# Kernel optimization log

Measured on AMD Instinct MI355X. Metric: run time of the kernel, lower is better.

## Reference

```python
import jax, jax.numpy as jnp
import numpy as np

N = 50000      # nodes
T = 4          # snapshots
F_IN = 128     # in_channels
H_DIM = 128    # hidden_channels
E = 800000     # edges per snapshot
K = 3          # Chebyshev order


def _edge_norm(src, dst, n):
    # PyG ChebConv sym normalization with lambda_max=2.0:
    # L_hat = L - I = -D^{-1/2} A D^{-1/2}  (diagonal of L_hat is 0)
    ones = jnp.ones(src.shape[0], jnp.float32)
    deg = jax.ops.segment_sum(ones, src, num_segments=n)
    dinv = jnp.where(deg > 0, jax.lax.rsqrt(deg), 0.0)
    return -dinv[src] * dinv[dst]


def _cheb_conv(x, src, dst, w, W, b):
    # x:(N,Fi), W:(K,Fi,Fo), b:(Fo,). Tx_0=x, Tx_1=L_hat x, Tx_k=2 L_hat Tx_{k-1} - Tx_{k-2}
    n = x.shape[0]

    def prop(t):  # sparse matmul L_hat @ t via gather-scale-scatter
        return jax.ops.segment_sum(w[:, None] * t[src], dst, num_segments=n)

    Tx0 = x
    out = Tx0 @ W[0]
    Tx1 = prop(Tx0)
    out = out + Tx1 @ W[1]
    for k in range(2, K):
        Tx2 = 2.0 * prop(Tx1) - Tx0
        out = out + Tx2 @ W[k]
        Tx0, Tx1 = Tx1, Tx2
    return out + b


def setup_inputs() -> dict:
    key = jax.random.key(0)
    ks = jax.random.split(key, 12)
    x = jax.random.normal(ks[0], (T, N, F_IN), jnp.float32)
    edge_index = jax.random.randint(ks[1], (T, 2, E), 0, N, dtype=jnp.int64)

    def w(k, fi, fo):
        return jax.random.normal(k, (K, fi, fo), jnp.float32) * 0.05

    inp = {
        "x": x, "edge_index": edge_index,
        "Wxz": w(ks[2], F_IN, H_DIM), "Whz": w(ks[3], H_DIM, H_DIM),
        "Wxr": w(ks[4], F_IN, H_DIM), "Whr": w(ks[5], H_DIM, H_DIM),
        "Wxh": w(ks[6], F_IN, H_DIM), "Whh": w(ks[7], H_DIM, H_DIM),
        "bxz": jnp.zeros(H_DIM, jnp.float32), "bhz": jnp.zeros(H_DIM, jnp.float32),
        "bxr": jnp.zeros(H_DIM, jnp.float32), "bhr": jnp.zeros(H_DIM, jnp.float32),
        "bxh": jnp.zeros(H_DIM, jnp.float32), "bhh": jnp.zeros(H_DIM, jnp.float32),
        "Wd1": jax.random.normal(ks[8], (H_DIM, H_DIM), jnp.float32) * 0.05,
        "bd1": jnp.zeros(H_DIM, jnp.float32),
        "Wd2": jax.random.normal(ks[9], (H_DIM, F_IN), jnp.float32) * 0.05,
        "bd2": jnp.zeros(F_IN, jnp.float32),
    }
    return inp


def reference(x, edge_index, Wxz, Whz, Wxr, Whr, Wxh, Whh,
              bxz, bhz, bxr, bhr, bxh, bhh, Wd1, bd1, Wd2, bd2):
    n = x.shape[1]

    def step(H, inp):
        xt, ei = inp
        src, dst = ei[0], ei[1]
        w = _edge_norm(src, dst, n)
        Z = jax.nn.sigmoid(_cheb_conv(xt, src, dst, w, Wxz, bxz)
                           + _cheb_conv(H, src, dst, w, Whz, bhz))
        R = jax.nn.sigmoid(_cheb_conv(xt, src, dst, w, Wxr, bxr)
                           + _cheb_conv(H, src, dst, w, Whr, bhr))
        Ht = jnp.tanh(_cheb_conv(xt, src, dst, w, Wxh, bxh)
                      + _cheb_conv(H * R, src, dst, w, Whh, bhh))
        H = Z * H + (1.0 - Z) * Ht
        return H, None

    H0 = jnp.zeros((n, H_DIM), x.dtype)
    H, _ = jax.lax.scan(step, H0, (x, edge_index))
    # decoder (dropout is identity at inference)
    x_pred = jax.nn.relu(H @ Wd1 + bd1) @ Wd2 + bd2
    return x_pred, H
```

## Files before the change

kernel.cpp:

```cpp
#include <hip/hip_runtime.h>
#include <math.h>

#define NN 50000
#define TT 4
#define FF 128
#define EE 800000
#define NSEG 4
#define BINSEG 12500
#define NCH 32
#define CHUNK 25000
#define NCH2 128
#define CH2 6250
#define NB2 64
#define CB 782
#define NSEG2 16
#define SEGW 3125
#define SBINS (CB*NSEG2)
#define SCHUNK 49
#define SMAX 13312

typedef __attribute__((ext_vector_type(8))) short bf8_t;
typedef __attribute__((ext_vector_type(4))) float f4_t;
typedef __attribute__((ext_vector_type(8))) ushort us8;

__device__ inline ushort f2bf(float f){
  union { float f; unsigned u; } v; v.f = f;
  unsigned u = v.u;
  unsigned r = (u + 0x7fff + ((u>>16)&1)) >> 16;
  return (ushort)r;
}
__device__ inline float lo16(unsigned u){ union{unsigned u;float f;}v; v.u=u<<16; return v.f; }
__device__ inline float hi16(unsigned u){ union{unsigned u;float f;}v; v.u=u&0xffff0000u; return v.f; }
__device__ inline unsigned packbf(float x, float y){
  return (unsigned)f2bf(x) | ((unsigned)f2bf(y)<<16);
}
__device__ inline float sigm(float x){ return 1.f/(1.f+expf(-x)); }

__global__ void k_cast4(const float* __restrict__ in, ushort* __restrict__ outp, int n4){
  int i = blockIdx.x*256 + threadIdx.x;
  if(i<n4){
    float4 v = ((const float4*)in)[i];
    ushort4 o; o.x=f2bf(v.x); o.y=f2bf(v.y); o.z=f2bf(v.z); o.w=f2bf(v.w);
    ((ushort4*)outp)[i]=o;
  }
}
__global__ void k_bias(const float* bxz, const float* bhz, const float* bxr,
                       const float* bhr, const float* bxh, const float* bhh,
                       float* __restrict__ bz, float* __restrict__ br, float* __restrict__ bh){
  int i = threadIdx.x;
  int c = i & 127, s = i >> 7;
  if(s==0) bz[c]=bxz[c]+bhz[c];
  else if(s==1) br[c]=bxr[c]+bhr[c];
  else bh[c]=bxh[c]+bhh[c];
}

__global__ __launch_bounds__(256) void k_hist(const int* __restrict__ ei,
                                              int* __restrict__ part){
  int c = blockIdx.x, seg = blockIdx.y, t = blockIdx.z;
  const int* keys = ei + (size_t)t*2*EE;
  __shared__ int h[BINSEG];
  for(int i=threadIdx.x;i<BINSEG;i+=256) h[i]=0;
  __syncthreads();
  int base = seg*BINSEG;
  int e0 = c*CHUNK, e1 = e0+CHUNK;
  for(int e=e0+threadIdx.x; e<e1; e+=256){
    int k = keys[e] - base;
    if((unsigned)k < (unsigned)BINSEG) atomicAdd(&h[k],1);
  }
  __syncthreads();
  int* dp = part + ((((size_t)t)*NSEG + seg)*NCH + c)*BINSEG;
  for(int i=threadIdx.x;i<BINSEG;i+=256) dp[i]=h[i];
}
__global__ void k_merge(const int* __restrict__ part, float* __restrict__ dinv4){
  int t = blockIdx.y;
  int n = blockIdx.x*256 + threadIdx.x;
  if(n>=NN) return;
  int seg = n / BINSEG, b = n - seg*BINSEG;
  const int* p = part + ((((size_t)t)*NSEG + seg)*NCH)*BINSEG + b;
  int s = 0;
  #pragma unroll
  for(int c=0;c<NCH;++c) s += p[(size_t)c*BINSEG];
  dinv4[(size_t)t*NN + n] = s>0 ? rsqrtf((float)s) : 0.f;
}

__global__ __launch_bounds__(256) void k_ccount(const int* __restrict__ ei,
                                                int* __restrict__ ccnt){
  int c = blockIdx.x, t = blockIdx.y;
  const int* dst = ei + (size_t)t*2*EE + EE;
  __shared__ int h[NB2];
  if(threadIdx.x<NB2) h[threadIdx.x]=0;
  __syncthreads();
  int e0 = c*CH2, e1 = e0+CH2;
  for(int e=e0+threadIdx.x; e<e1; e+=256) atomicAdd(&h[dst[e]/CB],1);
  __syncthreads();
  if(threadIdx.x<NB2) ccnt[((size_t)t*NB2 + threadIdx.x)*NCH2 + c] = h[threadIdx.x];
}
__global__ __launch_bounds__(128) void k_cscan(const int* __restrict__ ccnt,
                        int* __restrict__ Abase, int* __restrict__ Bbase,
                        int* __restrict__ tot){
  int t = blockIdx.x, tid = threadIdx.x;
  __shared__ int st[NB2];
  __shared__ int sb[NB2];
  const int* cc = ccnt + (size_t)t*NB2*NCH2;
  if(tid<NB2){
    int s=0;
    for(int c=0;c<NCH2;++c) s += cc[tid*NCH2+c];
    st[tid]=s;
  }
  __syncthreads();
  if(tid==0){
    int run=0;
    for(int b=0;b<NB2;++b){ sb[b]=run; run+=st[b]; }
  }
  __syncthreads();
  if(tid<NB2){
    Bbase[t*NB2+tid]=sb[tid];
    tot[t*NB2+tid]=st[tid];
    int run = sb[tid];
    int* ab = Abase + ((size_t)t*NB2 + tid)*NCH2;
    for(int c=0;c<NCH2;++c){ ab[c]=run; run+=cc[tid*NCH2+c]; }
  }
}
__global__ __launch_bounds__(256) void k_part(const int* __restrict__ ei,
                        const int* __restrict__ Abase, unsigned* __restrict__ staging){
  int c = blockIdx.x, t = blockIdx.y;
  const int* src = ei + (size_t)t*2*EE;
  const int* dst = src + EE;
  unsigned* stg = staging + (size_t)t*EE;
  const int* ab = Abase + (size_t)t*NB2*NCH2;
  __shared__ int h[NB2];
  if(threadIdx.x<NB2) h[threadIdx.x]=0;
  __syncthreads();
  int e0 = c*CH2, e1 = e0+CH2;
  for(int e=e0+threadIdx.x; e<e1; e+=256){
    int s=src[e], d=dst[e];
    int b = d/CB, dl = d - b*CB;
    int r = atomicAdd(&h[b],1);
    stg[ab[b*NCH2 + c] + r] = ((unsigned)dl<<16) | (unsigned)s;
  }
}
__global__ __launch_bounds__(256) void k_sortb(const unsigned* __restrict__ staging,
                        const int* __restrict__ Bbase, const int* __restrict__ tot,
                        const float* __restrict__ dinv4, int2* __restrict__ meta4,
                        int* __restrict__ offs4){
  int b = blockIdx.x, t = blockIdx.y, tid = threadIdx.x;
  __shared__ int cnt[SBINS];
  __shared__ int sums[256];
  __shared__ unsigned sorted[SMAX];
  int sA = Bbase[t*NB2+b];
  int nb = tot[t*NB2+b];
  const unsigned* stg = staging + (size_t)t*EE + sA;
  const float* dinv = dinv4 + (size_t)t*NN;
  int* offs = offs4 + (size_t)t*(NN+1);
  int2* meta = meta4 + (size_t)t*EE + sA;
  for(int i=tid;i<SBINS;i+=256) cnt[i]=0;
  __syncthreads();
  for(int i=tid;i<nb;i+=256){
    unsigned v = stg[i];
    int key = (int)(v>>16)*NSEG2 + (int)(v&0xFFFF)/SEGW;
    atomicAdd(&cnt[key],1);
  }
  __syncthreads();
  int base = tid*SCHUNK;
  int s0 = 0;
  for(int j=0;j<SCHUNK;++j){ int idx=base+j; if(idx<SBINS) s0+=cnt[idx]; }
  sums[tid]=s0; __syncthreads();
  for(int off=1;off<256;off<<=1){
    int v=(tid>=off)?sums[tid-off]:0; __syncthreads();
    sums[tid]+=v; __syncthreads();
  }
  int run = sums[tid]-s0;
  for(int j=0;j<SCHUNK;++j){
    int idx=base+j;
    if(idx<SBINS){ int c=cnt[idx]; cnt[idx]=run; run+=c; }
  }
  __syncthreads();
  for(int dl=tid; dl<CB; dl+=256){
    int n = b*CB + dl;
    if(n<=NN) offs[n] = sA + cnt[dl*NSEG2];
  }
  __syncthreads();
  for(int i=tid;i<nb;i+=256){
    unsigned v = stg[i];
    int key = (int)(v>>16)*NSEG2 + (int)(v&0xFFFF)/SEGW;
    int r = atomicAdd(&cnt[key],1);
    if(r<SMAX) sorted[r]=v;
  }
  __syncthreads();
  for(int i=tid;i<nb;i+=256){
    if(i>=SMAX) break;
    unsigned v = sorted[i];
    int s = v & 0xFFFF, d = b*CB + (v>>16);
    int2 m; m.x = s; m.y = __float_as_int(-dinv[s]*dinv[d]);
    meta[i]=m;
  }
}

__global__ void k_spmm2(const int* __restrict__ offs, const int2* __restrict__ meta,
                        const ushort* __restrict__ Xa, const ushort* __restrict__ Xb,
                        ushort* __restrict__ outA, ushort* __restrict__ outB){
  int wid = threadIdx.x>>6, lane = threadIdx.x&63;
  int row = blockIdx.x*4+wid;
  if(row>=NN) return;
  int beg = offs[row], end = offs[row+1];
  const unsigned* XA = (const unsigned*)Xa;
  const unsigned* XB = (const unsigned*)Xb;
  float ax=0.f, ay=0.f, bx=0.f, by=0.f;
  int e = beg;
  for(; e+3<end; e+=4){
    int2 p0=meta[e+0], p1=meta[e+1], p2=meta[e+2], p3=meta[e+3];
    float w0=__int_as_float(p0.y), w1=__int_as_float(p1.y);
    float w2=__int_as_float(p2.y), w3=__int_as_float(p3.y);
    unsigned a0=XA[p0.x*64+lane], a1=XA[p1.x*64+lane], a2=XA[p2.x*64+lane], a3=XA[p3.x*64+lane];
    unsigned b0=XB[p0.x*64+lane], b1=XB[p1.x*64+lane], b2=XB[p2.x*64+lane], b3=XB[p3.x*64+lane];
    ax=fmaf(w0,lo16(a0),ax); ay=fmaf(w0,hi16(a0),ay);
    ax=fmaf(w1,lo16(a1),ax); ay=fmaf(w1,hi16(a1),ay);
    ax=fmaf(w2,lo16(a2),ax); ay=fmaf(w2,hi16(a2),ay);
    ax=fmaf(w3,lo16(a3),ax); ay=fmaf(w3,hi16(a3),ay);
    bx=fmaf(w0,lo16(b0),bx); by=fmaf(w0,hi16(b0),by);
    bx=fmaf(w1,lo16(b1),bx); by=fmaf(w1,hi16(b1),by);
    bx=fmaf(w2,lo16(b2),bx); by=fmaf(w2,hi16(b2),by);
    bx=fmaf(w3,lo16(b3),bx); by=fmaf(w3,hi16(b3),by);
  }
  for(; e<end; ++e){
    int2 pm=meta[e]; float w=__int_as_float(pm.y);
    unsigned a=XA[pm.x*64+lane], b=XB[pm.x*64+lane];
    ax=fmaf(w,lo16(a),ax); ay=fmaf(w,hi16(a),ay);
    bx=fmaf(w,lo16(b),bx); by=fmaf(w,hi16(b),by);
  }
  int oi = row*64+lane;
  ((unsigned*)outA)[oi] = packbf(ax, ay);
  ((unsigned*)outB)[oi] = packbf(bx, by);
}
__global__ void k_spmm1(const int* __restrict__ offs, const int2* __restrict__ meta,
                        const ushort* __restrict__ Xa, ushort* __restrict__ outA){
  int wid = threadIdx.x>>6, lane = threadIdx.x&63;
  int row = blockIdx.x*4+wid;
  if(row>=NN) return;
  int beg = offs[row], end = offs[row+1];
  const unsigned* XA = (const unsigned*)Xa;
  float ax=0.f, ay=0.f;
  int e = beg;
  for(; e+3<end; e+=4){
    int2 p0=meta[e+0], p1=meta[e+1], p2=meta[e+2], p3=meta[e+3];
    float w0=__int_as_float(p0.y), w1=__int_as_float(p1.y);
    float w2=__int_as_float(p2.y), w3=__int_as_float(p3.y);
    unsigned a0=XA[p0.x*64+lane], a1=XA[p1.x*64+lane], a2=XA[p2.x*64+lane], a3=XA[p3.x*64+lane];
    ax=fmaf(w0,lo16(a0),ax); ay=fmaf(w0,hi16(a0),ay);
    ax=fmaf(w1,lo16(a1),ax); ay=fmaf(w1,hi16(a1),ay);
    ax=fmaf(w2,lo16(a2),ax); ay=fmaf(w2,hi16(a2),ay);
    ax=fmaf(w3,lo16(a3),ax); ay=fmaf(w3,hi16(a3),ay);
  }
  for(; e<end; ++e){
    int2 pm=meta[e]; float w=__int_as_float(pm.y);
    unsigned a=XA[pm.x*64+lane];
    ax=fmaf(w,lo16(a),ax); ay=fmaf(w,hi16(a),ay);
  }
  ((unsigned*)outA)[row*64+lane] = packbf(ax, ay);
}

__global__ __launch_bounds__(256) void k_mgemm(
    const ushort* __restrict__ A0, const ushort* __restrict__ A1,
    const ushort* __restrict__ A2, const ushort* __restrict__ A3,
    const ushort* __restrict__ A4, const ushort* __restrict__ A5,
    const ushort* __restrict__ Bt, ushort* __restrict__ Cb, float* __restrict__ Cf,
    int K, int ldb, int ngrp, int bnstep, int coloff, int mode, int nwg,
    const float* __restrict__ bias)
{
  __shared__ ushort As[128*64];
  __shared__ ushort Bs[128*64];
  int tid = threadIdx.x;
  int lane = tid & 63;
  int wid = tid >> 6;
  int wr = (wid>>1)*64, wc = (wid&1)*64;
  int bid = blockIdx.x;
  int q = nwg >> 3, r = nwg & 7;
  int xs = bid & 7, j = bid >> 3;
  int logical = xs*q + ((xs<r)?xs:r) + j;
  int bm = logical / ngrp;
  int bn = (logical - bm*ngrp) * bnstep;
  f4_t acc[4][4] = {};
  int srow = tid>>3, sc = tid&7;
  int lr = lane&15, lk = lane>>4;
  int nkt = K>>6;
  for(int kt=0; kt<nkt; ++kt){
    int k0 = kt<<6;
    const ushort* Ac = (k0<128)?A0:(k0<256)?A1:(k0<384)?A2:(k0<512)?A3:(k0<640)?A4:A5;
    int kloc = k0 & 127;
    #pragma unroll
    for(int p=0;p<4;++p){
      int rr = srow + p*32;
      int gr = bm*128 + rr; if(gr>=NN) gr=NN-1;
      us8 av = *(const us8*)(Ac + (size_t)gr*128 + kloc + sc*8);
      us8 bv = *(const us8*)(Bt + (size_t)(bn*128 + rr)*ldb + k0 + sc*8);
      int wo = (rr*128 + ((sc*16) ^ ((rr&7)<<4))) >> 1;
      *(us8*)(As + wo) = av;
      *(us8*)(Bs + wo) = bv;
    }
    __syncthreads();
    #pragma unroll
    for(int kk=0;kk<2;++kk){
      bf8_t af[4], bfr[4];
      int co = kk*64 + lk*16;
      #pragma unroll
      for(int m=0;m<4;++m){
        int Ra = wr + m*16 + lr;
        af[m]  = *(const bf8_t*)(As + ((Ra*128 + (co ^ ((Ra&7)<<4)))>>1));
        int Rb = wc + m*16 + lr;
        bfr[m] = *(const bf8_t*)(Bs + ((Rb*128 + (co ^ ((Rb&7)<<4)))>>1));
      }
      #pragma unroll
      for(int m=0;m<4;++m)
        #pragma unroll
        for(int n=0;n<4;++n)
          acc[m][n] = __builtin_amdgcn_mfma_f32_16x16x32_bf16(af[m], bfr[n], acc[m][n], 0,0,0);
    }
    __syncthreads();
  }
  int row0 = bm*128 + wr + lk*4;
  int col0 = bn*128 + wc + lr;
  #pragma unroll
  for(int m=0;m<4;++m){
    #pragma unroll
    for(int i=0;i<4;++i){
      int rI = row0 + m*16 + i;
      if(rI<NN){
        if(mode<=1){
          float* cp = Cf + (size_t)rI*384 + coloff + col0;
          #pragma unroll
          for(int n=0;n<4;++n){
            float v = acc[m][n][i];
            if(mode==1) v += cp[n*16];
            cp[n*16] = v;
          }
        } else if(mode==2){
          #pragma unroll
          for(int n=0;n<4;++n){
            int c = col0 + n*16;
            float v = acc[m][n][i] + bias[c];
            Cb[(size_t)rI*128 + c] = f2bf(fmaxf(v,0.f));
          }
        } else {
          #pragma unroll
          for(int n=0;n<4;++n){
            int c = col0 + n*16;
            Cf[(size_t)rI*128 + c] = acc[m][n][i] + bias[c];
          }
        }
      }
    }
  }
}

__global__ void k_combA(const float* __restrict__ OX, const float* __restrict__ H,
                        const float* __restrict__ bz, const float* __restrict__ br,
                        float* __restrict__ Z, ushort* __restrict__ HRb){
  int i = blockIdx.x*256 + threadIdx.x;
  if(i>=NN*FF) return;
  int r = i>>7, c = i&127;
  float zv = sigm(OX[r*384+c]     + bz[c]);
  float rv = sigm(OX[r*384+128+c] + br[c]);
  float hr = H[i]*rv;
  Z[i]=zv; HRb[i]=f2bf(hr);
}
__global__ void k_combB(const float* __restrict__ OX, const float* __restrict__ Z,
                        const float* __restrict__ H, const float* __restrict__ bh,
                        float* __restrict__ Hn, ushort* __restrict__ Hnb,
                        float* __restrict__ Hout2){
  int i = blockIdx.x*256 + threadIdx.x;
  if(i>=NN*FF) return;
  int r = i>>7, c = i&127;
  float ht = tanhf(OX[r*384+256+c] + bh[c]);
  float z = Z[i];
  float hn = z*H[i] + (1.f-z)*ht;
  Hn[i] = hn; Hnb[i] = f2bf(hn);
  if(Hout2) Hout2[i] = hn;
}
__global__ void k_gru0(const float* __restrict__ OX, const float* __restrict__ bz,
                       const float* __restrict__ bh, float* __restrict__ Hn,
                       ushort* __restrict__ Hnb){
  int i = blockIdx.x*256 + threadIdx.x;
  if(i>=NN*FF) return;
  int r = i>>7, c = i&127;
  float z  = sigm(OX[r*384+c] + bz[c]);
  float ht = tanhf(OX[r*384+256+c] + bh[c]);
  float hn = (1.f - z)*ht;
  Hn[i]=hn; Hnb[i]=f2bf(hn);
}

__global__ void k_packx(const float* __restrict__ Wxz, const float* __restrict__ Wxr,
                        const float* __restrict__ Wxh, const float* __restrict__ Whz,
                        const float* __restrict__ Whr, ushort* __restrict__ Bt){
  int i = blockIdx.x*256 + threadIdx.x;
  if(i>=384*768) return;
  int c = i/768, k = i - c*768;
  int g = c>>7, j = c&127;
  int kb = k>>7, kk = k&127;
  float v;
  int e = kk*128 + j;
  if(kb<3){
    const float* W = (g==0)?Wxz:((g==1)?Wxr:Wxh);
    v = (kb==0) ? (W[e] - W[2*16384 + e]) : (kb==1 ? W[16384 + e] : 2.f*W[2*16384 + e]);
  } else if(g<2){
    const float* W = (g==0)?Whz:Whr;
    int kb2 = kb-3;
    v = (kb2==0) ? (W[e] - W[2*16384 + e]) : (kb2==1 ? W[16384 + e] : 2.f*W[2*16384 + e]);
  } else v = 0.f;
  Bt[i] = f2bf(v);
}
__global__ void k_packh(const float* __restrict__ Whh, ushort* __restrict__ Bt){
  int i = blockIdx.x*256 + threadIdx.x;
  if(i>=128*384) return;
  int c = i/384, k = i - c*384;
  int kb = k>>7, kk = k&127;
  int e = kk*128 + c;
  float v = (kb==0) ? (Whh[e] - Whh[2*16384 + e]) : (kb==1 ? Whh[16384 + e] : 2.f*Whh[2*16384 + e]);
  Bt[i] = f2bf(v);
}
__global__ void k_packd(const float* __restrict__ W, ushort* __restrict__ Bt){
  int i = blockIdx.x*256 + threadIdx.x;
  if(i>=128*128) return;
  int c = i>>7, k = i&127;
  Bt[i] = f2bf(W[k*128 + c]);
}

extern "C" void kernel_launch(void* const* d_in, const int* in_sizes, int n_in,
                              void* d_out, int out_size, void* d_ws, size_t ws_size,
                              hipStream_t stream) {
  const float* x   = (const float*)d_in[0];
  const int*   ei  = (const int*)d_in[1];
  const float* Wxz = (const float*)d_in[2];
  const float* Whz = (const float*)d_in[3];
  const float* Wxr = (const float*)d_in[4];
  const float* Whr = (const float*)d_in[5];
  const float* Wxh = (const float*)d_in[6];
  const float* Whh = (const float*)d_in[7];
  const float* bxz = (const float*)d_in[8];
  const float* bhz = (const float*)d_in[9];
  const float* bxr = (const float*)d_in[10];
  const float* bhr = (const float*)d_in[11];
  const float* bxh = (const float*)d_in[12];
  const float* bhh = (const float*)d_in[13];
  const float* Wd1 = (const float*)d_in[14];
  const float* bd1 = (const float*)d_in[15];
  const float* Wd2 = (const float*)d_in[16];
  const float* bd2 = (const float*)d_in[17];
  float* out = (float*)d_out;

  char* p = (char*)d_ws;
  auto alloc = [&](size_t bytes)->void*{ void* r = (void*)p; p += (bytes+255)&~(size_t)255; return r; };
  const size_t NFB  = (size_t)NN*FF*4;
  const size_t NFB2 = (size_t)NN*FF*2;
  float* Ha   = (float*)alloc(NFB);
  float* Hb   = (float*)alloc(NFB);
  float* OX   = (float*)alloc((size_t)NN*384*4);
  float* Zb   = (float*)alloc(NFB);
  ushort* xtb4= (ushort*)alloc(NFB2*TT);
  ushort* A1b = (ushort*)alloc(NFB2);
  ushort* A2b = (ushort*)alloc(NFB2);
  ushort* A3b = (ushort*)alloc(NFB2);
  ushort* A4b = (ushort*)alloc(NFB2);
  ushort* HRb = (ushort*)alloc(NFB2);
  ushort* Hab = (ushort*)alloc(NFB2);
  ushort* Hbb = (ushort*)alloc(NFB2);
  ushort* Btx = (ushort*)alloc((size_t)384*768*2);
  ushort* Bth = (ushort*)alloc((size_t)128*384*2);
  ushort* Btd1= (ushort*)alloc((size_t)128*128*2);
  ushort* Btd2= (ushort*)alloc((size_t)128*128*2);
  float* bzc  = (float*)alloc(128*4);
  float* brc  = (float*)alloc(128*4);
  float* bhc  = (float*)alloc(128*4);
  float* dinv4= (float*)alloc((size_t)TT*NN*4);
  int* ccnt   = (int*)alloc((size_t)TT*NB2*NCH2*4);
  int* Abase  = (int*)alloc((size_t)TT*NB2*NCH2*4);
  int* Bbase  = (int*)alloc((size_t)TT*NB2*4);
  int* tot    = (int*)alloc((size_t)TT*NB2*4);
  int* offs4  = (int*)alloc((size_t)TT*(NN+1)*4);
  int2* meta4 = (int2*)alloc((size_t)TT*EE*8);
  int* partial = (int*)Ha;
  unsigned* staging = (unsigned*)Hb;

  const int fb = (NN*FF+255)/256;
  const int sg = (NN+3)/4;
  const int MT = (NN+127)/128;

  k_packx<<<(384*768+255)/256,256,0,stream>>>(Wxz,Wxr,Wxh,Whz,Whr,Btx);
  k_packh<<<(128*384+255)/256,256,0,stream>>>(Whh,Bth);
  k_packd<<<64,256,0,stream>>>(Wd1,Btd1);
  k_packd<<<64,256,0,stream>>>(Wd2,Btd2);
  k_bias<<<1,384,0,stream>>>(bxz,bhz,bxr,bhr,bxh,bhh,bzc,brc,bhc);
  k_cast4<<<(TT*NN*FF/4+255)/256,256,0,stream>>>(x, xtb4, TT*NN*FF/4);
  dim3 gh(NCH, NSEG, TT);
  k_hist<<<gh,256,0,stream>>>(ei, partial);
  dim3 gm((NN+255)/256, TT);
  k_merge<<<gm,256,0,stream>>>(partial, dinv4);
  dim3 gc(NCH2, TT);
  k_ccount<<<gc,256,0,stream>>>(ei, ccnt);
  k_cscan<<<TT,128,0,stream>>>(ccnt, Abase, Bbase, tot);
  k_part<<<gc,256,0,stream>>>(ei, Abase, staging);
  dim3 gs(NB2, TT);
  k_sortb<<<gs,256,0,stream>>>(staging, Bbase, tot, dinv4, meta4, offs4);

  float* Hc = Ha; float* Hn = Hb;
  ushort* Hcb = Hab; ushort* Hnb = Hbb;
  for(int t=0;t<TT;++t){
    const ushort* xtb = xtb4 + (size_t)t*NN*FF;
    const int* offs = offs4 + (size_t)t*(NN+1);
    const int2* meta = meta4 + (size_t)t*EE;
    if(t==0){
      k_spmm1<<<sg,256,0,stream>>>(offs,meta, xtb, A1b);
      k_spmm1<<<sg,256,0,stream>>>(offs,meta, A1b, A2b);
      int nwg0 = MT*2;
      k_mgemm<<<nwg0,256,0,stream>>>(xtb,A1b,A2b,nullptr,nullptr,nullptr,
          Btx, nullptr, OX, 384, 768, 2, 2, 0, 0, nwg0, nullptr);
      k_gru0<<<fb,256,0,stream>>>(OX, bzc, bhc, Hn, Hnb);
    } else {
      k_spmm2<<<sg,256,0,stream>>>(offs,meta, xtb,Hcb, A1b,A3b);
      k_spmm2<<<sg,256,0,stream>>>(offs,meta, A1b,A3b, A2b,A4b);
      int nwg1 = MT*3;
      k_mgemm<<<nwg1,256,0,stream>>>(xtb,A1b,A2b,Hcb,A3b,A4b,
          Btx, nullptr, OX, 768, 768, 3, 1, 0, 0, nwg1, nullptr);
      k_combA<<<fb,256,0,stream>>>(OX,Hc,bzc,brc,Zb,HRb);
      k_spmm1<<<sg,256,0,stream>>>(offs,meta, HRb, A3b);
      k_spmm1<<<sg,256,0,stream>>>(offs,meta, A3b, A4b);
      int nwg3 = MT;
      k_mgemm<<<nwg3,256,0,stream>>>(HRb,A3b,A4b,nullptr,nullptr,nullptr,
          Bth, nullptr, OX, 384, 384, 1, 1, 256, 1, nwg3, nullptr);
      float* hout2 = (t==TT-1) ? (out + (size_t)NN*FF) : nullptr;
      k_combB<<<fb,256,0,stream>>>(OX,Zb,Hc,bhc,Hn,Hnb,hout2);
    }
    float* tmp=Hc; Hc=Hn; Hn=tmp;
    ushort* tb=Hcb; Hcb=Hnb; Hnb=tb;
  }
  k_mgemm<<<MT,256,0,stream>>>(Hcb,nullptr,nullptr,nullptr,nullptr,nullptr,
      Btd1, A1b, nullptr, 128, 128, 1, 1, 0, 2, MT, bd1);
  k_mgemm<<<MT,256,0,stream>>>(A1b,nullptr,nullptr,nullptr,nullptr,nullptr,
      Btd2, nullptr, out, 128, 128, 1, 1, 0, 3, MT, bd2);
}
```

Measured before the change: 1.257 ms.

## Store bf16 features in column-quarter-major layout and split SpMM by feature quarter

```diff
diff --git a/kernel.cpp b/kernel.cpp
--- a/kernel.cpp
+++ b/kernel.cpp
@@ -18,6 +18,7 @@
 #define SBINS (CB*NSEG2)
 #define SCHUNK 49
 #define SMAX 13312
+#define SPB 2048
 
 typedef __attribute__((ext_vector_type(8))) short bf8_t;
 typedef __attribute__((ext_vector_type(4))) float f4_t;
@@ -36,12 +37,17 @@
 }
 __device__ inline float sigm(float x){ return 1.f/(1.f+expf(-x)); }
 
+
 __global__ void k_cast4(const float* __restrict__ in, ushort* __restrict__ outp, int n4){
   int i = blockIdx.x*256 + threadIdx.x;
   if(i<n4){
     float4 v = ((const float4*)in)[i];
     ushort4 o; o.x=f2bf(v.x); o.y=f2bf(v.y); o.z=f2bf(v.z); o.w=f2bf(v.w);
-    ((ushort4*)outp)[i]=o;
+    int t = i / (NN*32);
+    int rem = i - t*(NN*32);
+    int r = rem >> 5;
+    int f = (rem & 31) * 4;
+    *(ushort4*)(outp + (size_t)t*NN*128 + ((size_t)(f>>5)*NN + r)*32 + (f&31)) = o;
   }
 }
 __global__ void k_bias(const float* bxz, const float* bhz, const float* bxr,
@@ -196,67 +202,80 @@
   }
 }
 
-__global__ void k_spmm2(const int* __restrict__ offs, const int2* __restrict__ meta,
+__global__ __launch_bounds__(256) void k_spmm2q(const int* __restrict__ offs,
+                        const int2* __restrict__ meta,
                         const ushort* __restrict__ Xa, const ushort* __restrict__ Xb,
                         ushort* __restrict__ outA, ushort* __restrict__ outB){
-  int wid = threadIdx.x>>6, lane = threadIdx.x&63;
-  int row = blockIdx.x*4+wid;
-  if(row>=NN) return;
-  int beg = offs[row], end = offs[row+1];
-  const unsigned* XA = (const unsigned*)Xa;
-  const unsigned* XB = (const unsigned*)Xb;
-  float ax=0.f, ay=0.f, bx=0.f, by=0.f;
-  int e = beg;
-  for(; e+3<end; e+=4){
-    int2 p0=meta[e+0], p1=meta[e+1], p2=meta[e+2], p3=meta[e+3];
-    float w0=__int_as_float(p0.y), w1=__int_as_float(p1.y);
-    float w2=__int_as_float(p2.y), w3=__int_as_float(p3.y);
-    unsigned a0=XA[p0.x*64+lane], a1=XA[p1.x*64+lane], a2=XA[p2.x*64+lane], a3=XA[p3.x*64+lane];
-    unsigned b0=XB[p0.x*64+lane], b1=XB[p1.x*64+lane], b2=XB[p2.x*64+lane], b3=XB[p3.x*64+lane];
-    ax=fmaf(w0,lo16(a0),ax); ay=fmaf(w0,hi16(a0),ay);
-    ax=fmaf(w1,lo16(a1),ax); ay=fmaf(w1,hi16(a1),ay);
-    ax=fmaf(w2,lo16(a2),ax); ay=fmaf(w2,hi16(a2),ay);
-    ax=fmaf(w3,lo16(a3),ax); ay=fmaf(w3,hi16(a3),ay);
-    bx=fmaf(w0,lo16(b0),bx); by=fmaf(w0,hi16(b0),by);
-    bx=fmaf(w1,lo16(b1),bx); by=fmaf(w1,hi16(b1),by);
-    bx=fmaf(w2,lo16(b2),bx); by=fmaf(w2,hi16(b2),by);
-    bx=fmaf(w3,lo16(b3),bx); by=fmaf(w3,hi16(b3),by);
-  }
-  for(; e<end; ++e){
-    int2 pm=meta[e]; float w=__int_as_float(pm.y);
-    unsigned a=XA[pm.x*64+lane], b=XB[pm.x*64+lane];
-    ax=fmaf(w,lo16(a),ax); ay=fmaf(w,hi16(a),ay);
-    bx=fmaf(w,lo16(b),bx); by=fmaf(w,hi16(b),by);
-  }
-  int oi = row*64+lane;
-  ((unsigned*)outA)[oi] = packbf(ax, ay);
-  ((unsigned*)outB)[oi] = packbf(bx, by);
-}
-__global__ void k_spmm1(const int* __restrict__ offs, const int2* __restrict__ meta,
+  int bid = blockIdx.x;
+  int q = (bid & 7) >> 1;
+  int rank = ((bid >> 3) << 1) | (bid & 1);
+  int g = threadIdx.x >> 4, l = threadIdx.x & 15;
+  const unsigned* XA = (const unsigned*)Xa + (size_t)q*NN*16;
+  const unsigned* XB = (const unsigned*)Xb + (size_t)q*NN*16;
+  unsigned* OA = (unsigned*)outA + (size_t)q*NN*16;
+  unsigned* OB = (unsigned*)outB + (size_t)q*NN*16;
+  for(int row = rank*16 + g; row < NN; row += (SPB/4)*16){
+    int beg = offs[row], end = offs[row+1];
+    float ax=0.f, ay=0.f, bx=0.f, by=0.f;
+    int e = beg;
+    for(; e+3<end; e+=4){
+      int2 p0=meta[e+0], p1=meta[e+1], p2=meta[e+2], p3=meta[e+3];
+      float w0=__int_as_float(p0.y), w1=__int_as_float(p1.y);
+      float w2=__int_as_float(p2.y), w3=__int_as_float(p3.y);
+      unsigned a0=XA[(size_t)p0.x*16+l], a1=XA[(size_t)p1.x*16+l];
+      unsigned a2=XA[(size_t)p2.x*16+l], a3=XA[(size_t)p3.x*16+l];
+      unsigned b0=XB[(size_t)p0.x*16+l], b1=XB[(size_t)p1.x*16+l];
+      unsigned b2=XB[(size_t)p2.x*16+l], b3=XB[(size_t)p3.x*16+l];
+      ax=fmaf(w0,lo16(a0),ax); ay=fmaf(w0,hi16(a0),ay);
+      ax=fmaf(w1,lo16(a1),ax); ay=fmaf(w1,hi16(a1),ay);
+      ax=fmaf(w2,lo16(a2),ax); ay=fmaf(w2,hi16(a2),ay);
+      ax=fmaf(w3,lo16(a3),ax); ay=fmaf(w3,hi16(a3),ay);
+      bx=fmaf(w0,lo16(b0),bx); by=fmaf(w0,hi16(b0),by);
+      bx=fmaf(w1,lo16(b1),bx); by=fmaf(w1,hi16(b1),by);
+      bx=fmaf(w2,lo16(b2),bx); by=fmaf(w2,hi16(b2),by);
+      bx=fmaf(w3,lo16(b3),bx); by=fmaf(w3,hi16(b3),by);
+    }
+    for(; e<end; ++e){
+      int2 pm=meta[e]; float w=__int_as_float(pm.y);
+      unsigned a=XA[(size_t)pm.x*16+l], b=XB[(size_t)pm.x*16+l];
+      ax=fmaf(w,lo16(a),ax); ay=fmaf(w,hi16(a),ay);
+      bx=fmaf(w,lo16(b),bx); by=fmaf(w,hi16(b),by);
+    }
+    OA[(size_t)row*16 + l] = packbf(ax, ay);
+    OB[(size_t)row*16 + l] = packbf(bx, by);
+  }
+}
+__global__ __launch_bounds__(256) void k_spmm1q(const int* __restrict__ offs,
+                        const int2* __restrict__ meta,
                         const ushort* __restrict__ Xa, ushort* __restrict__ outA){
-  int wid = threadIdx.x>>6, lane = threadIdx.x&63;
-  int row = blockIdx.x*4+wid;
-  if(row>=NN) return;
-  int beg = offs[row], end = offs[row+1];
-  const unsigned* XA = (const unsigned*)Xa;
-  float ax=0.f, ay=0.f;
-  int e = beg;
-  for(; e+3<end; e+=4){
-    int2 p0=meta[e+0], p1=meta[e+1], p2=meta[e+2], p3=meta[e+3];
-    float w0=__int_as_float(p0.y), w1=__int_as_float(p1.y);
-    float w2=__int_as_float(p2.y), w3=__int_as_float(p3.y);
-    unsigned a0=XA[p0.x*64+lane], a1=XA[p1.x*64+lane], a2=XA[p2.x*64+lane], a3=XA[p3.x*64+lane];
-    ax=fmaf(w0,lo16(a0),ax); ay=fmaf(w0,hi16(a0),ay);
-    ax=fmaf(w1,lo16(a1),ax); ay=fmaf(w1,hi16(a1),ay);
-    ax=fmaf(w2,lo16(a2),ax); ay=fmaf(w2,hi16(a2),ay);
-    ax=fmaf(w3,lo16(a3),ax); ay=fmaf(w3,hi16(a3),ay);
-  }
-  for(; e<end; ++e){
-    int2 pm=meta[e]; float w=__int_as_float(pm.y);
-    unsigned a=XA[pm.x*64+lane];
-    ax=fmaf(w,lo16(a),ax); ay=fmaf(w,hi16(a),ay);
-  }
-  ((unsigned*)outA)[row*64+lane] = packbf(ax, ay);
+  int bid = blockIdx.x;
+  int q = (bid & 7) >> 1;
+  int rank = ((bid >> 3) << 1) | (bid & 1);
+  int g = threadIdx.x >> 4, l = threadIdx.x & 15;
+  const unsigned* XA = (const unsigned*)Xa + (size_t)q*NN*16;
+  unsigned* OA = (unsigned*)outA + (size_t)q*NN*16;
+  for(int row = rank*16 + g; row < NN; row += (SPB/4)*16){
+    int beg = offs[row], end = offs[row+1];
+    float ax=0.f, ay=0.f;
+    int e = beg;
+    for(; e+3<end; e+=4){
+      int2 p0=meta[e+0], p1=meta[e+1], p2=meta[e+2], p3=meta[e+3];
+      float w0=__int_as_float(p0.y), w1=__int_as_float(p1.y);
+      float w2=__int_as_float(p2.y), w3=__int_as_float(p3.y);
+      unsigned a0=XA[(size_t)p0.x*16+l], a1=XA[(size_t)p1.x*16+l];
+      unsigned a2=XA[(size_t)p2.x*16+l], a3=XA[(size_t)p3.x*16+l];
+      ax=fmaf(w0,lo16(a0),ax); ay=fmaf(w0,hi16(a0),ay);
+      ax=fmaf(w1,lo16(a1),ax); ay=fmaf(w1,hi16(a1),ay);
+      ax=fmaf(w2,lo16(a2),ax); ay=fmaf(w2,hi16(a2),ay);
+      ax=fmaf(w3,lo16(a3),ax); ay=fmaf(w3,hi16(a3),ay);
+    }
+    for(; e<end; ++e){
+      int2 pm=meta[e]; float w=__int_as_float(pm.y);
+      unsigned a=XA[(size_t)pm.x*16+l];
+      ax=fmaf(w,lo16(a),ax); ay=fmaf(w,hi16(a),ay);
+    }
+    OA[(size_t)row*16 + l] = packbf(ax, ay);
+  }
 }
 
 __global__ __launch_bounds__(256) void k_mgemm(
@@ -287,11 +306,13 @@
     int k0 = kt<<6;
     const ushort* Ac = (k0<128)?A0:(k0<256)?A1:(k0<384)?A2:(k0<512)?A3:(k0<640)?A4:A5;
     int kloc = k0 & 127;
+    int f0 = kloc + sc*8;
+    size_t aoff = ((size_t)(f0>>5)*NN)*32 + (f0&31);
     #pragma unroll
     for(int p=0;p<4;++p){
       int rr = srow + p*32;
       int gr = bm*128 + rr; if(gr>=NN) gr=NN-1;
-      us8 av = *(const us8*)(Ac + (size_t)gr*128 + kloc + sc*8);
+      us8 av = *(const us8*)(Ac + aoff + (size_t)gr*32);
       us8 bv = *(const us8*)(Bt + (size_t)(bn*128 + rr)*ldb + k0 + sc*8);
       int wo = (rr*128 + ((sc*16) ^ ((rr&7)<<4))) >> 1;
       *(us8*)(As + wo) = av;
@@ -338,7 +359,7 @@
           for(int n=0;n<4;++n){
             int c = col0 + n*16;
             float v = acc[m][n][i] + bias[c];
-            Cb[(size_t)rI*128 + c] = f2bf(fmaxf(v,0.f));
+            Cb[((size_t)(c>>5)*NN + rI)*32 + (c&31)] = f2bf(fmaxf(v,0.f));
           }
         } else {
           #pragma unroll
@@ -361,7 +382,8 @@
   float zv = sigm(OX[r*384+c]     + bz[c]);
   float rv = sigm(OX[r*384+128+c] + br[c]);
   float hr = H[i]*rv;
-  Z[i]=zv; HRb[i]=f2bf(hr);
+  Z[i]=zv;
+  HRb[((size_t)(c>>5)*NN + r)*32 + (c&31)] = f2bf(hr);
 }
 __global__ void k_combB(const float* __restrict__ OX, const float* __restrict__ Z,
                         const float* __restrict__ H, const float* __restrict__ bh,
@@ -373,7 +395,8 @@
   float ht = tanhf(OX[r*384+256+c] + bh[c]);
   float z = Z[i];
   float hn = z*H[i] + (1.f-z)*ht;
-  Hn[i] = hn; Hnb[i] = f2bf(hn);
+  Hn[i] = hn;
+  Hnb[((size_t)(c>>5)*NN + r)*32 + (c&31)] = f2bf(hn);
   if(Hout2) Hout2[i] = hn;
 }
 __global__ void k_gru0(const float* __restrict__ OX, const float* __restrict__ bz,
@@ -385,7 +408,8 @@
   float z  = sigm(OX[r*384+c] + bz[c]);
   float ht = tanhf(OX[r*384+256+c] + bh[c]);
   float hn = (1.f - z)*ht;
-  Hn[i]=hn; Hnb[i]=f2bf(hn);
+  Hn[i]=hn;
+  Hnb[((size_t)(c>>5)*NN + r)*32 + (c&31)] = f2bf(hn);
 }
 
 __global__ void k_packx(const float* __restrict__ Wxz, const float* __restrict__ Wxr,
@@ -481,7 +505,6 @@
   unsigned* staging = (unsigned*)Hb;
 
   const int fb = (NN*FF+255)/256;
-  const int sg = (NN+3)/4;
   const int MT = (NN+127)/128;
 
   k_packx<<<(384*768+255)/256,256,0,stream>>>(Wxz,Wxr,Wxh,Whz,Whr,Btx);
@@ -508,21 +531,21 @@
     const int* offs = offs4 + (size_t)t*(NN+1);
     const int2* meta = meta4 + (size_t)t*EE;
     if(t==0){
-      k_spmm1<<<sg,256,0,stream>>>(offs,meta, xtb, A1b);
-      k_spmm1<<<sg,256,0,stream>>>(offs,meta, A1b, A2b);
+      k_spmm1q<<<SPB,256,0,stream>>>(offs,meta, xtb, A1b);
+      k_spmm1q<<<SPB,256,0,stream>>>(offs,meta, A1b, A2b);
       int nwg0 = MT*2;
       k_mgemm<<<nwg0,256,0,stream>>>(xtb,A1b,A2b,nullptr,nullptr,nullptr,
           Btx, nullptr, OX, 384, 768, 2, 2, 0, 0, nwg0, nullptr);
       k_gru0<<<fb,256,0,stream>>>(OX, bzc, bhc, Hn, Hnb);
     } else {
-      k_spmm2<<<sg,256,0,stream>>>(offs,meta, xtb,Hcb, A1b,A3b);
-      k_spmm2<<<sg,256,0,stream>>>(offs,meta, A1b,A3b, A2b,A4b);
+      k_spmm2q<<<SPB,256,0,stream>>>(offs,meta, xtb,Hcb, A1b,A3b);
+      k_spmm2q<<<SPB,256,0,stream>>>(offs,meta, A1b,A3b, A2b,A4b);
       int nwg1 = MT*3;
       k_mgemm<<<nwg1,256,0,stream>>>(xtb,A1b,A2b,Hcb,A3b,A4b,
           Btx, nullptr, OX, 768, 768, 3, 1, 0, 0, nwg1, nullptr);
       k_combA<<<fb,256,0,stream>>>(OX,Hc,bzc,brc,Zb,HRb);
-      k_spmm1<<<sg,256,0,stream>>>(offs,meta, HRb, A3b);
-      k_spmm1<<<sg,256,0,stream>>>(offs,meta, A3b, A4b);
+      k_spmm1q<<<SPB,256,0,stream>>>(offs,meta, HRb, A3b);
+      k_spmm1q<<<SPB,256,0,stream>>>(offs,meta, A3b, A4b);
       int nwg3 = MT;
       k_mgemm<<<nwg3,256,0,stream>>>(HRb,A3b,A4b,nullptr,nullptr,nullptr,
           Bth, nullptr, OX, 384, 384, 1, 1, 256, 1, nwg3, nullptr);
```

Result: slower. 1.355 ms (+7.9%).
